# Kernel optimization log

Hardware: AMD Instinct MI355X
Metric: run time of the kernel (lower is better)

## Reference

```python
import jax, jax.numpy as jnp
import numpy as np

N = 50000
E = 800000
EC = 200000
L = 128
PD = 3
IN_MAIN = 2 * L + 2 * (PD + 1)   # 264
IN_CONT = 2 * L + PD + 1          # 260
IN_NODE = 3 * L                   # 384
EPS = 1e-5


def _ln(h):
    # LayerNorm over last dim, no affine params
    m = jnp.mean(h, axis=-1, keepdims=True)
    v = jnp.mean(jnp.square(h - m), axis=-1, keepdims=True)
    return (h - m) * jax.lax.rsqrt(v + EPS)


def _mlp(h, W0, b0, W1, b1, W2, b2):
    # 2 hidden ReLU layers + output Linear + LayerNorm(no affine)
    h = jax.nn.relu(h @ W0 + b0)
    h = jax.nn.relu(h @ W1 + b1)
    return _ln(h @ W2 + b2)


def _mp(x, idx, pos, pos_w, use_mat, W0, b0, W1, b1, W2, b2):
    i, j = idx[0], idx[1]
    x_i = x[i]
    x_j = x[j]
    feats = []
    if use_mat:
        d = pos[i] - pos[j]
        feats += [d, jnp.linalg.norm(d, axis=-1, keepdims=True)]
    dw = pos_w[i] - pos_w[j]
    feats += [dw, jnp.linalg.norm(dw, axis=-1, keepdims=True)]
    tmp = jnp.concatenate(feats + [x_i, x_j], axis=-1)
    emb = _mlp(tmp, W0, b0, W1, b1, W2, b2)
    return jax.ops.segment_sum(emb, j, num_segments=N)


def _lin(key, fan_in, fan_out):
    k1, k2 = jax.random.split(key)
    bd = 1.0 / np.sqrt(fan_in)
    W = jax.random.uniform(k1, (fan_in, fan_out), jnp.float32, -bd, bd)
    b = jax.random.uniform(k2, (fan_out,), jnp.float32, -bd, bd)
    return W, b


def setup_inputs() -> dict:
    key = jax.random.key(0)
    ks = jax.random.split(key, 16)
    inp = {
        "x": jax.random.normal(ks[0], (N, L), jnp.float32),
        "g": jax.random.randint(ks[1], (2, E), 0, N, jnp.int32),
        "cg": jax.random.randint(ks[2], (2, EC), 0, N, jnp.int32),
        "pos_posw": jax.random.normal(ks[3], (N, 2 * PD), jnp.float32),
    }
    dims = {"main": IN_MAIN, "cont": IN_CONT, "node": IN_NODE}
    kidx = 4
    for name, in_dim in dims.items():
        fi = in_dim
        for l in range(3):
            W, b = _lin(ks[kidx], fi, L)
            inp[f"{name}_W{l}"] = W
            inp[f"{name}_b{l}"] = b
            fi = L
            kidx += 1
    return inp


def reference(x, g, cg, pos_posw,
              main_W0, main_b0, main_W1, main_b1, main_W2, main_b2,
              cont_W0, cont_b0, cont_W1, cont_b1, cont_W2, cont_b2,
              node_W0, node_b0, node_W1, node_b1, node_W2, node_b2):
    D = pos_posw.shape[-1] // 2
    pos, pos_w = pos_posw[:, :D], pos_posw[:, D:]
    agg_main = _mp(x, g, pos, pos_w, True,
                   main_W0, main_b0, main_W1, main_b1, main_W2, main_b2)
    agg_cont = _mp(x, cg, pos, pos_w, False,
                   cont_W0, cont_b0, cont_W1, cont_b1, cont_W2, cont_b2)
    tmp = jnp.concatenate([x, agg_main, agg_cont], axis=-1)
    return _mlp(tmp, node_W0, node_b0, node_W1, node_b1, node_W2, node_b2) + x
```

## Files before the change

### kernel.cpp

```cpp
#include <hip/hip_runtime.h>

#define NN 50000
#define NE_MAIN 800000
#define NE_CONT 200000
#define NP 50176

typedef __attribute__((ext_vector_type(8))) short bf8;
typedef __attribute__((ext_vector_type(4))) float f4;

static __device__ __forceinline__ float bf2f(short s) {
  return __builtin_bit_cast(float, ((unsigned int)(unsigned short)s) << 16);
}
static __device__ __forceinline__ short f2bf(float f) {
  unsigned int u = __builtin_bit_cast(unsigned int, f);
  u += 0x7fffu + ((u >> 16) & 1u);
  return (short)(u >> 16);
}

static __device__ __forceinline__ int xcd_swizzle(int bid, int nwg) {
  int xcd = bid & 7;
  int q = nwg >> 3, r = nwg & 7;
  int base = (xcd < r) ? xcd * (q + 1) : r * (q + 1) + (xcd - r) * q;
  return base + (bid >> 3);
}

__global__ __launch_bounds__(256) void zero_kernel(f4* __restrict__ p, int n4) {
  int i = blockIdx.x * 256 + threadIdx.x;
  int stride = gridDim.x * 256;
  f4 z = {0.f, 0.f, 0.f, 0.f};
  for (; i < n4; i += stride) p[i] = z;
}

__global__ __launch_bounds__(256) void hist_kernel(const int* __restrict__ idx, int nE,
                                                   int* __restrict__ hist) {
  int e = blockIdx.x * 256 + threadIdx.x;
  int st = gridDim.x * 256;
  for (; e < nE; e += st) atomicAdd(&hist[idx[nE + e]], 1);
}

__global__ __launch_bounds__(512) void scan1_kernel(const int* __restrict__ hist,
                                                    int* __restrict__ cursor,
                                                    int* __restrict__ tsums, int n) {
  __shared__ int buf[2][512];
  int tid = threadIdx.x;
  int i = blockIdx.x * 512 + tid;
  int v = (i < n) ? hist[i] : 0;
  int cur = 0;
  buf[0][tid] = v;
  __syncthreads();
#pragma unroll
  for (int off = 1; off < 512; off <<= 1) {
    int t = buf[cur][tid];
    if (tid >= off) t += buf[cur][tid - off];
    buf[cur ^ 1][tid] = t;
    cur ^= 1;
    __syncthreads();
  }
  int incl = buf[cur][tid];
  if (i < n) cursor[i] = incl - v;
  if (tid == 511) tsums[blockIdx.x] = incl;
}

__global__ __launch_bounds__(512) void scan2_kernel(int* __restrict__ tsums, int nt) {
  __shared__ int buf[2][512];
  int tid = threadIdx.x;
  int v = (tid < nt) ? tsums[tid] : 0;
  int cur = 0;
  buf[0][tid] = v;
  __syncthreads();
#pragma unroll
  for (int off = 1; off < 512; off <<= 1) {
    int t = buf[cur][tid];
    if (tid >= off) t += buf[cur][tid - off];
    buf[cur ^ 1][tid] = t;
    cur ^= 1;
    __syncthreads();
  }
  if (tid < nt) tsums[tid] = buf[cur][tid] - v;
}

__global__ __launch_bounds__(512) void scan3_kernel(int* __restrict__ cursor,
                                                    const int* __restrict__ tsums, int n) {
  int i = blockIdx.x * 512 + threadIdx.x;
  if (i < n) cursor[i] += tsums[blockIdx.x];
}

__global__ __launch_bounds__(256) void scatter_kernel(const int* __restrict__ idx, int nE,
                                                      int* __restrict__ cursor,
                                                      int* __restrict__ si, int* __restrict__ sj) {
  int e = blockIdx.x * 256 + threadIdx.x;
  int st = gridDim.x * 256;
  for (; e < nE; e += st) {
    int i = idx[e], j = idx[nE + e];
    int p = atomicAdd(&cursor[j], 1);
    si[p] = i;
    sj[p] = j;
  }
}

struct WTDesc {
  const float* src[11];
  int K[11];
  int off[11];
};
__global__ __launch_bounds__(128) void wt_kernel(WTDesc d, short* __restrict__ dst) {
  int m = blockIdx.x >> 7;
  int n = blockIdx.x & 127;
  const float* s = d.src[m];
  int K = d.K[m];
  short* o = dst + d.off[m] + (size_t)n * K;
  for (int k = threadIdx.x; k < K; k += 128) o[k] = f2bf(s[(size_t)k * 128 + n]);
}

template <int K>
static __device__ __forceinline__ void mfma_gemm(const short* __restrict__ sA, int rs16,
                                                 const short* __restrict__ WT,
                                                 int c0, int lane,
                                                 const float* __restrict__ bias,
                                                 f4 (&acc)[4][2]) {
  const int colA = c0 + (lane & 15);
  const int colB = colA + 16;
  if (bias) {
    float ba = bias[colA], bb = bias[colB];
#pragma unroll
    for (int rf = 0; rf < 4; ++rf) {
      acc[rf][0] = (f4){ba, ba, ba, ba};
      acc[rf][1] = (f4){bb, bb, bb, bb};
    }
  } else {
#pragma unroll
    for (int rf = 0; rf < 4; ++rf) {
      acc[rf][0] = (f4){0.f, 0.f, 0.f, 0.f};
      acc[rf][1] = (f4){0.f, 0.f, 0.f, 0.f};
    }
  }
  const int g = lane >> 4;
  const int rowl = lane & 15;
#pragma unroll 4
  for (int ks = 0; ks < (K >> 5); ++ks) {
    bf8 b0 = *reinterpret_cast<const bf8*>(WT + (size_t)colA * K + ks * 32 + g * 8);
    bf8 b1 = *reinterpret_cast<const bf8*>(WT + (size_t)colB * K + ks * 32 + g * 8);
    int chunk = ks * 4 + g;
#pragma unroll
    for (int rf = 0; rf < 4; ++rf) {
      int row = rf * 16 + rowl;
      bf8 a = *reinterpret_cast<const bf8*>(sA + row * rs16 * 8 + ((chunk ^ (row & 7)) << 3));
      acc[rf][0] = __builtin_amdgcn_mfma_f32_16x16x32_bf16(a, b0, acc[rf][0], 0, 0, 0);
      acc[rf][1] = __builtin_amdgcn_mfma_f32_16x16x32_bf16(a, b1, acc[rf][1], 0, 0, 0);
    }
  }
}

template <bool RELU, bool SWZ>
static __device__ __forceinline__ void store_frags(short* __restrict__ dst, int rs16,
                                                   int c0, int lane, const f4 (&acc)[4][2]) {
#pragma unroll
  for (int rf = 0; rf < 4; ++rf)
#pragma unroll
    for (int q = 0; q < 4; ++q) {
      int row = rf * 16 + ((lane >> 4) << 2) + q;
#pragma unroll
      for (int cf = 0; cf < 2; ++cf) {
        int col = c0 + cf * 16 + (lane & 15);
        float v = acc[rf][cf][q];
        if (RELU) v = fmaxf(v, 0.f);
        int idx;
        if (SWZ) idx = row * rs16 * 8 + (((col >> 3) ^ (row & 7)) << 3) + (col & 7);
        else     idx = row * rs16 * 8 + col;
        dst[idx] = f2bf(v);
      }
    }
}

static __device__ __forceinline__ void ln_rows(const f4 (&acc)[4][2], int lane, int wave,
                                               float2* __restrict__ sP) {
#pragma unroll
  for (int rf = 0; rf < 4; ++rf)
#pragma unroll
    for (int q = 0; q < 4; ++q) {
      float v0 = acc[rf][0][q], v1 = acc[rf][1][q];
      float s = v0 + v1;
      float qq = v0 * v0 + v1 * v1;
      s += __shfl_xor(s, 1);  qq += __shfl_xor(qq, 1);
      s += __shfl_xor(s, 2);  qq += __shfl_xor(qq, 2);
      s += __shfl_xor(s, 4);  qq += __shfl_xor(qq, 4);
      s += __shfl_xor(s, 8);  qq += __shfl_xor(qq, 8);
      if ((lane & 15) == 0) {
        int row = rf * 16 + ((lane >> 4) << 2) + q;
        sP[wave * 64 + row] = make_float2(s, qq);
      }
    }
}

__global__ __launch_bounds__(256) void precompute_kernel(
    const float* __restrict__ x, const short* __restrict__ WTp,
    short* __restrict__ xa_m, short* __restrict__ xb_m,
    short* __restrict__ xa_c, short* __restrict__ xb_c) {
  __shared__ __align__(16) short sA[64 * 128];
  __shared__ __align__(16) short sOut[64 * 128];
  const int tid = threadIdx.x;
  const int lane = tid & 63, wave = tid >> 6;
  const int c0 = wave * 32;
  const int n0 = blockIdx.x * 64;

#pragma unroll
  for (int it = 0; it < 4; ++it) {
    int s = it * 256 + tid;
    int e = s >> 4, c = s & 15;
    int n = n0 + e;
    f4 u0 = {0.f, 0.f, 0.f, 0.f}, u1 = {0.f, 0.f, 0.f, 0.f};
    if (n < NN) {
      u0 = *reinterpret_cast<const f4*>(x + (size_t)n * 128 + c * 8);
      u1 = *reinterpret_cast<const f4*>(x + (size_t)n * 128 + c * 8 + 4);
    }
    bf8 o;
#pragma unroll
    for (int j = 0; j < 4; ++j) { o[j] = f2bf(u0[j]); o[j + 4] = f2bf(u1[j]); }
    *reinterpret_cast<bf8*>(sA + e * 128 + ((c ^ (e & 7)) << 3)) = o;
  }
  __syncthreads();

  short* dsts[4] = {xa_m, xb_m, xa_c, xb_c};
#pragma unroll 1
  for (int o = 0; o < 4; ++o) {
    f4 acc[4][2];
    mfma_gemm<128>(sA, 16, WTp + o * 16384, c0, lane, nullptr, acc);
    store_frags<false, false>(sOut, 16, c0, lane, acc);
    __syncthreads();
    short* dst = dsts[o];
#pragma unroll
    for (int it = 0; it < 4; ++it) {
      int s = it * 256 + tid;
      int e = s >> 4, c = s & 15;
      int n = n0 + e;
      if (n < NN)
        *reinterpret_cast<bf8*>(dst + (size_t)n * 128 + c * 8) =
            *reinterpret_cast<const bf8*>(sOut + e * 128 + c * 8);
    }
    __syncthreads();
  }
}

template <int NF>
__global__ __launch_bounds__(256) void edge_kernel(
    const int* __restrict__ si, const int* __restrict__ sjv, int nE,
    const float* __restrict__ pp,
    const short* __restrict__ xa, const short* __restrict__ xb,
    const float* __restrict__ W0f, const float* __restrict__ b0v,
    const short* __restrict__ WT1, const float* __restrict__ b1v,
    const short* __restrict__ WT2, const float* __restrict__ b2v,
    float* __restrict__ agg) {
  __shared__ __align__(16) short sAB[2 * 64 * 128];
  __shared__ int sI[64], sJ[64];
  __shared__ float sF[64][NF];
  __shared__ float2 sP[4 * 64];
  __shared__ float2 sStats[64];
  const int tid = threadIdx.x;
  const int lane = tid & 63, wave = tid >> 6;
  const int c0 = wave * 32;
  const int base = xcd_swizzle(blockIdx.x, gridDim.x) * 64;
  short* sA = sAB;
  short* sB = sAB + 64 * 128;
  float* sT = reinterpret_cast<float*>(sAB);

  if (tid < 64) {
    int e = base + tid;
    int i = si[e];
    int j = sjv[e];
    sI[tid] = i; sJ[tid] = j;
    const float* pi = pp + (size_t)i * 6;
    const float* pj = pp + (size_t)j * 6;
    if (NF == 8) {
      float d0 = pi[0] - pj[0], d1 = pi[1] - pj[1], d2 = pi[2] - pj[2];
      sF[tid][0] = d0; sF[tid][1] = d1; sF[tid][2] = d2;
      sF[tid][3] = sqrtf(d0 * d0 + d1 * d1 + d2 * d2);
      float w0 = pi[3] - pj[3], w1 = pi[4] - pj[4], w2 = pi[5] - pj[5];
      sF[tid][4] = w0; sF[tid][5] = w1; sF[tid][6] = w2;
      sF[tid][7] = sqrtf(w0 * w0 + w1 * w1 + w2 * w2);
    } else {
      float w0 = pi[3] - pj[3], w1 = pi[4] - pj[4], w2 = pi[5] - pj[5];
      sF[tid][0] = w0; sF[tid][1] = w1; sF[tid][2] = w2;
      sF[tid][3] = sqrtf(w0 * w0 + w1 * w1 + w2 * w2);
    }
  }
  __syncthreads();

#pragma unroll
  for (int it = 0; it < 4; ++it) {
    int s = it * 256 + tid;
    int e = s >> 4, c = s & 15;
    int i = sI[e], j = sJ[e];
    bf8 va = *reinterpret_cast<const bf8*>(xa + (size_t)i * 128 + c * 8);
    bf8 vb = *reinterpret_cast<const bf8*>(xb + (size_t)j * 128 + c * 8);
    f4 b0a = *reinterpret_cast<const f4*>(b0v + c * 8);
    f4 b0b = *reinterpret_cast<const f4*>(b0v + c * 8 + 4);
    float h[8];
#pragma unroll
    for (int jj = 0; jj < 4; ++jj) {
      h[jj]     = bf2f(va[jj])     + bf2f(vb[jj])     + b0a[jj];
      h[jj + 4] = bf2f(va[jj + 4]) + bf2f(vb[jj + 4]) + b0b[jj];
    }
#pragma unroll
    for (int q = 0; q < NF; ++q) {
      float fq = sF[e][q];
      f4 w0 = *reinterpret_cast<const f4*>(W0f + q * 128 + c * 8);
      f4 w1 = *reinterpret_cast<const f4*>(W0f + q * 128 + c * 8 + 4);
#pragma unroll
      for (int jj = 0; jj < 4; ++jj) {
        h[jj]     = fmaf(fq, w0[jj], h[jj]);
        h[jj + 4] = fmaf(fq, w1[jj], h[jj + 4]);
      }
    }
    bf8 o;
#pragma unroll
    for (int jj = 0; jj < 8; ++jj) o[jj] = f2bf(fmaxf(h[jj], 0.f));
    *reinterpret_cast<bf8*>(sA + e * 128 + ((c ^ (e & 7)) << 3)) = o;
  }
  __syncthreads();

  f4 acc[4][2];
  mfma_gemm<128>(sA, 16, WT1, c0, lane, b1v, acc);
  store_frags<true, true>(sB, 16, c0, lane, acc);
  __syncthreads();
  mfma_gemm<128>(sB, 16, WT2, c0, lane, b2v, acc);

  ln_rows(acc, lane, wave, sP);
  __syncthreads();
  if (tid < 64) {
    float s = 0.f, qq = 0.f;
#pragma unroll
    for (int w = 0; w < 4; ++w) { s += sP[w * 64 + tid].x; qq += sP[w * 64 + tid].y; }
    float mean = s * (1.f / 128.f);
    float var = qq * (1.f / 128.f) - mean * mean;
    sStats[tid] = make_float2(mean, rsqrtf(var + 1e-5f));
  }
  __syncthreads();

#pragma unroll
  for (int rf = 0; rf < 4; ++rf)
#pragma unroll
    for (int q = 0; q < 4; ++q) {
      int row = rf * 16 + ((lane >> 4) << 2) + q;
      float mean = sStats[row].x, rn = sStats[row].y;
#pragma unroll
      for (int cf = 0; cf < 2; ++cf) {
        int col = c0 + cf * 16 + (lane & 15);
        sT[row * 128 + col] = (acc[rf][cf][q] - mean) * rn;
      }
    }
  __syncthreads();

  {
    int grp = tid >> 7, c = tid & 127;
    int r0 = grp * 32;
    float accum = 0.f;
#pragma unroll 4
    for (int r = r0; r < r0 + 32; ++r) {
      accum += sT[r * 128 + c];
      bool flush = (r == r0 + 31) || (sJ[r + 1] != sJ[r]);
      if (flush) {
        unsafeAtomicAdd(agg + (size_t)sJ[r] * 128 + c, accum);
        accum = 0.f;
      }
    }
  }
}

__global__ __launch_bounds__(256) void node_kernel(
    const float* __restrict__ x,
    const float* __restrict__ agg_m, const float* __restrict__ agg_c,
    const short* __restrict__ WT0, const float* __restrict__ b0v,
    const short* __restrict__ WT1, const float* __restrict__ b1v,
    const short* __restrict__ WT2, const float* __restrict__ b2v,
    float* __restrict__ out) {
  __shared__ __align__(16) short sA[64 * 384];
  __shared__ float2 sP[4 * 64];
  __shared__ float2 sStats[64];
  const int tid = threadIdx.x;
  const int lane = tid & 63, wave = tid >> 6;
  const int c0 = wave * 32;
  const int n0 = blockIdx.x * 64;

#pragma unroll
  for (int p = 0; p < 3; ++p) {
    const float* src = (p == 0) ? x : (p == 1) ? agg_m : agg_c;
#pragma unroll
    for (int it = 0; it < 4; ++it) {
      int s = it * 256 + tid;
      int e = s >> 4, cl = s & 15;
      int n = n0 + e;
      f4 u0 = {0.f, 0.f, 0.f, 0.f}, u1 = {0.f, 0.f, 0.f, 0.f};
      if (n < NN) {
        u0 = *reinterpret_cast<const f4*>(src + (size_t)n * 128 + cl * 8);
        u1 = *reinterpret_cast<const f4*>(src + (size_t)n * 128 + cl * 8 + 4);
      }
      bf8 o;
#pragma unroll
      for (int j = 0; j < 4; ++j) { o[j] = f2bf(u0[j]); o[j + 4] = f2bf(u1[j]); }
      int c = p * 16 + cl;
      *reinterpret_cast<bf8*>(sA + e * 384 + ((c ^ (e & 7)) << 3)) = o;
    }
  }
  __syncthreads();

  f4 acc[4][2];
  mfma_gemm<384>(sA, 48, WT0, c0, lane, b0v, acc);
  __syncthreads();
  store_frags<true, true>(sA, 16, c0, lane, acc);
  __syncthreads();
  mfma_gemm<128>(sA, 16, WT1, c0, lane, b1v, acc);
  __syncthreads();
  store_frags<true, true>(sA + 8192, 16, c0, lane, acc);
  __syncthreads();
  mfma_gemm<128>(sA + 8192, 16, WT2, c0, lane, b2v, acc);

  ln_rows(acc, lane, wave, sP);
  __syncthreads();
  if (tid < 64) {
    float s = 0.f, qq = 0.f;
#pragma unroll
    for (int w = 0; w < 4; ++w) { s += sP[w * 64 + tid].x; qq += sP[w * 64 + tid].y; }
    float mean = s * (1.f / 128.f);
    float var = qq * (1.f / 128.f) - mean * mean;
    sStats[tid] = make_float2(mean, rsqrtf(var + 1e-5f));
  }
  __syncthreads();

#pragma unroll
  for (int rf = 0; rf < 4; ++rf)
#pragma unroll
    for (int q = 0; q < 4; ++q) {
      int row = rf * 16 + ((lane >> 4) << 2) + q;
      int n = n0 + row;
      if (n < NN) {
        float mean = sStats[row].x, rn = sStats[row].y;
#pragma unroll
        for (int cf = 0; cf < 2; ++cf) {
          int col = c0 + cf * 16 + (lane & 15);
          float xv = x[(size_t)n * 128 + col];
          out[(size_t)n * 128 + col] = (acc[rf][cf][q] - mean) * rn + xv;
        }
      }
    }
}

extern "C" void kernel_launch(void* const* d_in, const int* in_sizes, int n_in,
                              void* d_out, int out_size, void* d_ws, size_t ws_size,
                              hipStream_t stream) {
  const float* x   = (const float*)d_in[0];
  const int*   g   = (const int*)d_in[1];
  const int*   cgr = (const int*)d_in[2];
  const float* pp  = (const float*)d_in[3];
  const float* mW0 = (const float*)d_in[4];
  const float* mb0 = (const float*)d_in[5];
  const float* mW1 = (const float*)d_in[6];
  const float* mb1 = (const float*)d_in[7];
  const float* mW2 = (const float*)d_in[8];
  const float* mb2 = (const float*)d_in[9];
  const float* cW0 = (const float*)d_in[10];
  const float* cb0 = (const float*)d_in[11];
  const float* cW1 = (const float*)d_in[12];
  const float* cb1 = (const float*)d_in[13];
  const float* cW2 = (const float*)d_in[14];
  const float* cb2 = (const float*)d_in[15];
  const float* nW0 = (const float*)d_in[16];
  const float* nb0 = (const float*)d_in[17];
  const float* nW1 = (const float*)d_in[18];
  const float* nb1 = (const float*)d_in[19];
  const float* nW2 = (const float*)d_in[20];
  const float* nb2 = (const float*)d_in[21];
  float* out = (float*)d_out;

  WTDesc d;
  const float* srcs[11] = {mW1, mW2, cW1, cW2, nW0, nW1, nW2,
                           mW0 + 8 * 128, mW0 + 136 * 128, cW0 + 4 * 128, cW0 + 132 * 128};
  int Ks[11] = {128, 128, 128, 128, 384, 128, 128, 128, 128, 128, 128};
  int off = 0;
  for (int m = 0; m < 11; ++m) { d.src[m] = srcs[m]; d.K[m] = Ks[m]; d.off[m] = off; off += Ks[m] * 128; }

  char* ws = (char*)d_ws;
  const size_t TBL = (size_t)NN * 128 * 2;
  const size_t AGG = (size_t)NN * 128 * 4;
  short* xa_m = (short*)(ws);
  short* xb_m = (short*)(ws + TBL);
  short* xa_c = (short*)(ws + 2 * TBL);
  short* xb_c = (short*)(ws + 3 * TBL);
  float* agg_m = (float*)(ws + 4 * TBL);
  float* agg_c = (float*)(ws + 4 * TBL + AGG);
  short* wt = (short*)(ws + 4 * TBL + 2 * AGG);
  char* ib = ws + 4 * TBL + 2 * AGG + (size_t)off * 2;
  int* hist_m   = (int*)(ib);
  int* hist_c   = hist_m + NP;
  int* cursor_m = hist_c + NP;
  int* cursor_c = cursor_m + NP;
  int* tsum_m   = cursor_c + NP;
  int* tsum_c   = tsum_m + 128;
  int* si_m     = tsum_c + 128;
  int* sj_m     = si_m + NE_MAIN;
  int* si_c     = sj_m + NE_MAIN;
  int* sj_c     = si_c + NE_CONT;

  short* wt1_m = wt + d.off[0];
  short* wt2_m = wt + d.off[1];
  short* wt1_c = wt + d.off[2];
  short* wt2_c = wt + d.off[3];
  short* wtn0  = wt + d.off[4];
  short* wtn1  = wt + d.off[5];
  short* wtn2  = wt + d.off[6];
  short* wtp   = wt + d.off[7];

  const int NT = (NN + 511) / 512;

  wt_kernel<<<11 * 128, 128, 0, stream>>>(d, wt);
  zero_kernel<<<2048, 256, 0, stream>>>((f4*)agg_m, (int)(2 * (size_t)NN * 128 / 4));
  zero_kernel<<<128, 256, 0, stream>>>((f4*)hist_m, 2 * NP / 4);

  hist_kernel<<<1024, 256, 0, stream>>>(g, NE_MAIN, hist_m);
  hist_kernel<<<512, 256, 0, stream>>>(cgr, NE_CONT, hist_c);
  scan1_kernel<<<NT, 512, 0, stream>>>(hist_m, cursor_m, tsum_m, NN);
  scan1_kernel<<<NT, 512, 0, stream>>>(hist_c, cursor_c, tsum_c, NN);
  scan2_kernel<<<1, 512, 0, stream>>>(tsum_m, NT);
  scan2_kernel<<<1, 512, 0, stream>>>(tsum_c, NT);
  scan3_kernel<<<NT, 512, 0, stream>>>(cursor_m, tsum_m, NN);
  scan3_kernel<<<NT, 512, 0, stream>>>(cursor_c, tsum_c, NN);
  scatter_kernel<<<1024, 256, 0, stream>>>(g, NE_MAIN, cursor_m, si_m, sj_m);
  scatter_kernel<<<512, 256, 0, stream>>>(cgr, NE_CONT, cursor_c, si_c, sj_c);

  precompute_kernel<<<(NN + 63) / 64, 256, 0, stream>>>(x, wtp, xa_m, xb_m, xa_c, xb_c);
  edge_kernel<8><<<NE_MAIN / 64, 256, 0, stream>>>(si_m, sj_m, NE_MAIN, pp, xa_m, xb_m,
                                                   mW0, mb0, wt1_m, mb1, wt2_m, mb2, agg_m);
  edge_kernel<4><<<NE_CONT / 64, 256, 0, stream>>>(si_c, sj_c, NE_CONT, pp, xa_c, xb_c,
                                                   cW0, cb0, wt1_c, cb1, wt2_c, cb2, agg_c);
  node_kernel<<<(NN + 63) / 64, 256, 0, stream>>>(x, agg_m, agg_c,
                                                  wtn0, nb0, wtn1, nb1, wtn2, nb2, out);
}
```

Before: 670.6 us.

## Fuse edge kernels into persistent kernel with prefetched gathers and bias folding

Result: slower. 1.097 ms (+63.5%).

```diff
diff --git a/kernel.cpp b/kernel.cpp
--- a/kernel.cpp
+++ b/kernel.cpp
@@ -1,9 +1,12 @@
 #include <hip/hip_runtime.h>
+#include <hip/hip_bf16.h>
 
 #define NN 50000
 #define NE_MAIN 800000
 #define NE_CONT 200000
 #define NP 50176
+#define BLK_M 768
+#define BLK_C 192
 
 typedef __attribute__((ext_vector_type(8))) short bf8;
 typedef __attribute__((ext_vector_type(4))) float f4;
@@ -12,16 +15,8 @@
   return __builtin_bit_cast(float, ((unsigned int)(unsigned short)s) << 16);
 }
 static __device__ __forceinline__ short f2bf(float f) {
-  unsigned int u = __builtin_bit_cast(unsigned int, f);
-  u += 0x7fffu + ((u >> 16) & 1u);
-  return (short)(u >> 16);
-}
-
-static __device__ __forceinline__ int xcd_swizzle(int bid, int nwg) {
-  int xcd = bid & 7;
-  int q = nwg >> 3, r = nwg & 7;
-  int base = (xcd < r) ? xcd * (q + 1) : r * (q + 1) + (xcd - r) * q;
-  return base + (bid >> 3);
+  __hip_bfloat16 h = __float2bfloat16(f);
+  return __builtin_bit_cast(short, h);
 }
 
 __global__ __launch_bounds__(256) void zero_kernel(f4* __restrict__ p, int n4) {
@@ -194,6 +189,7 @@
 
 __global__ __launch_bounds__(256) void precompute_kernel(
     const float* __restrict__ x, const short* __restrict__ WTp,
+    const float* __restrict__ mb0, const float* __restrict__ cb0,
     short* __restrict__ xa_m, short* __restrict__ xb_m,
     short* __restrict__ xa_c, short* __restrict__ xb_c) {
   __shared__ __align__(16) short sA[64 * 128];
@@ -221,10 +217,11 @@
   __syncthreads();
 
   short* dsts[4] = {xa_m, xb_m, xa_c, xb_c};
+  const float* biases[4] = {nullptr, mb0, nullptr, cb0};
 #pragma unroll 1
   for (int o = 0; o < 4; ++o) {
     f4 acc[4][2];
-    mfma_gemm<128>(sA, 16, WTp + o * 16384, c0, lane, nullptr, acc);
+    mfma_gemm<128>(sA, 16, WTp + o * 16384, c0, lane, biases[o], acc);
     store_frags<false, false>(sOut, 16, c0, lane, acc);
     __syncthreads();
     short* dst = dsts[o];
@@ -241,128 +238,180 @@
   }
 }
 
+struct EdgeArgs {
+  const int* si; const int* sj;
+  const short* xa; const short* xb;
+  const float* pp;
+  const float* W0f;
+  const short* WT1; const float* b1;
+  const short* WT2; const float* b2;
+  float* agg;
+  int ntiles; int nblocks; int nf;
+};
+
 template <int NF>
-__global__ __launch_bounds__(256) void edge_kernel(
-    const int* __restrict__ si, const int* __restrict__ sjv, int nE,
-    const float* __restrict__ pp,
-    const short* __restrict__ xa, const short* __restrict__ xb,
-    const float* __restrict__ W0f, const float* __restrict__ b0v,
-    const short* __restrict__ WT1, const float* __restrict__ b1v,
-    const short* __restrict__ WT2, const float* __restrict__ b2v,
-    float* __restrict__ agg) {
+static __device__ __forceinline__ void stage_h0(short* __restrict__ sA,
+                                                const bf8 (&pxa)[4], const bf8 (&pxb)[4],
+                                                const float (* __restrict__ sFc)[8],
+                                                const float* __restrict__ W0f, int tid) {
+#pragma unroll
+  for (int it = 0; it < 4; ++it) {
+    int s = it * 256 + tid;
+    int e = s >> 4, c = s & 15;
+    float h[8];
+#pragma unroll
+    for (int jj = 0; jj < 8; ++jj) h[jj] = bf2f(pxa[it][jj]) + bf2f(pxb[it][jj]);
+#pragma unroll
+    for (int q = 0; q < NF; ++q) {
+      float fq = sFc[e][q];
+      f4 w0 = *reinterpret_cast<const f4*>(W0f + q * 128 + c * 8);
+      f4 w1 = *reinterpret_cast<const f4*>(W0f + q * 128 + c * 8 + 4);
+#pragma unroll
+      for (int jj = 0; jj < 4; ++jj) {
+        h[jj]     = fmaf(fq, w0[jj], h[jj]);
+        h[jj + 4] = fmaf(fq, w1[jj], h[jj + 4]);
+      }
+    }
+    bf8 o;
+#pragma unroll
+    for (int jj = 0; jj < 8; ++jj) o[jj] = f2bf(fmaxf(h[jj], 0.f));
+    *reinterpret_cast<bf8*>(sA + e * 128 + ((c ^ (e & 7)) << 3)) = o;
+  }
+}
+
+__global__ __launch_bounds__(256, 4) void edge_fused_kernel(EdgeArgs am, EdgeArgs ac,
+                                                            int blocks_m) {
   __shared__ __align__(16) short sAB[2 * 64 * 128];
-  __shared__ int sI[64], sJ[64];
-  __shared__ float sF[64][NF];
+  __shared__ int sI[2][64], sJ[2][64];
+  __shared__ float sF[2][64][8];
   __shared__ float2 sP[4 * 64];
   __shared__ float2 sStats[64];
   const int tid = threadIdx.x;
   const int lane = tid & 63, wave = tid >> 6;
   const int c0 = wave * 32;
-  const int base = xcd_swizzle(blockIdx.x, gridDim.x) * 64;
   short* sA = sAB;
   short* sB = sAB + 64 * 128;
   float* sT = reinterpret_cast<float*>(sAB);
 
+  EdgeArgs A;
+  int lb;
+  if ((int)blockIdx.x < blocks_m) { A = am; lb = blockIdx.x; }
+  else                            { A = ac; lb = blockIdx.x - blocks_m; }
+  const int per = A.nblocks >> 3;
+  lb = (lb & 7) * per + (lb >> 3);
+  const int q = A.ntiles / A.nblocks, r = A.ntiles % A.nblocks;
+  const int t0 = lb * q + (lb < r ? lb : r);
+  const int t1 = t0 + q + (lb < r ? 1 : 0);
+  if (t0 >= t1) return;
+  const int nf = A.nf;
+
+  int cur = 0;
   if (tid < 64) {
-    int e = base + tid;
-    int i = si[e];
-    int j = sjv[e];
-    sI[tid] = i; sJ[tid] = j;
-    const float* pi = pp + (size_t)i * 6;
-    const float* pj = pp + (size_t)j * 6;
-    if (NF == 8) {
+    int e = t0 * 64 + tid;
+    int i = A.si[e], j = A.sj[e];
+    sI[0][tid] = i; sJ[0][tid] = j;
+    const float* pi = A.pp + (size_t)i * 6;
+    const float* pj = A.pp + (size_t)j * 6;
+    float d0 = pi[0] - pj[0], d1 = pi[1] - pj[1], d2 = pi[2] - pj[2];
+    float w0 = pi[3] - pj[3], w1 = pi[4] - pj[4], w2 = pi[5] - pj[5];
+    float* sf = sF[0][tid];
+    if (nf == 8) {
+      sf[0] = d0; sf[1] = d1; sf[2] = d2; sf[3] = sqrtf(d0 * d0 + d1 * d1 + d2 * d2);
+      sf[4] = w0; sf[5] = w1; sf[6] = w2; sf[7] = sqrtf(w0 * w0 + w1 * w1 + w2 * w2);
+    } else {
+      sf[0] = w0; sf[1] = w1; sf[2] = w2; sf[3] = sqrtf(w0 * w0 + w1 * w1 + w2 * w2);
+    }
+  }
+  __syncthreads();
+
+  bf8 pxa[4], pxb[4];
+#pragma unroll
+  for (int it = 0; it < 4; ++it) {
+    int s = it * 256 + tid, e = s >> 4, c = s & 15;
+    pxa[it] = *reinterpret_cast<const bf8*>(A.xa + (size_t)sI[0][e] * 128 + c * 8);
+    pxb[it] = *reinterpret_cast<const bf8*>(A.xb + (size_t)sJ[0][e] * 128 + c * 8);
+  }
+
+  for (int tt = t0; tt < t1; ++tt) {
+    const bool nb = (tt + 1 < t1);
+    int ni = 0, nj2 = 0;
+    if (nb && tid < 64) {
+      int e = (tt + 1) * 64 + tid;
+      ni = A.si[e];
+      nj2 = A.sj[e];
+    }
+    if (nf == 8) stage_h0<8>(sA, pxa, pxb, sF[cur], A.W0f, tid);
+    else         stage_h0<4>(sA, pxa, pxb, sF[cur], A.W0f, tid);
+    __syncthreads();
+    if (nb && tid < 64) {
+      int nxt = cur ^ 1;
+      sI[nxt][tid] = ni; sJ[nxt][tid] = nj2;
+      const float* pi = A.pp + (size_t)ni * 6;
+      const float* pj = A.pp + (size_t)nj2 * 6;
       float d0 = pi[0] - pj[0], d1 = pi[1] - pj[1], d2 = pi[2] - pj[2];
-      sF[tid][0] = d0; sF[tid][1] = d1; sF[tid][2] = d2;
-      sF[tid][3] = sqrtf(d0 * d0 + d1 * d1 + d2 * d2);
       float w0 = pi[3] - pj[3], w1 = pi[4] - pj[4], w2 = pi[5] - pj[5];
-      sF[tid][4] = w0; sF[tid][5] = w1; sF[tid][6] = w2;
-      sF[tid][7] = sqrtf(w0 * w0 + w1 * w1 + w2 * w2);
-    } else {
-      float w0 = pi[3] - pj[3], w1 = pi[4] - pj[4], w2 = pi[5] - pj[5];
-      sF[tid][0] = w0; sF[tid][1] = w1; sF[tid][2] = w2;
-      sF[tid][3] = sqrtf(w0 * w0 + w1 * w1 + w2 * w2);
-    }
-  }
-  __syncthreads();
-
-#pragma unroll
-  for (int it = 0; it < 4; ++it) {
-    int s = it * 256 + tid;
-    int e = s >> 4, c = s & 15;
-    int i = sI[e], j = sJ[e];
-    bf8 va = *reinterpret_cast<const bf8*>(xa + (size_t)i * 128 + c * 8);
-    bf8 vb = *reinterpret_cast<const bf8*>(xb + (size_t)j * 128 + c * 8);
-    f4 b0a = *reinterpret_cast<const f4*>(b0v + c * 8);
-    f4 b0b = *reinterpret_cast<const f4*>(b0v + c * 8 + 4);
-    float h[8];
-#pragma unroll
-    for (int jj = 0; jj < 4; ++jj) {
-      h[jj]     = bf2f(va[jj])     + bf2f(vb[jj])     + b0a[jj];
-      h[jj + 4] = bf2f(va[jj + 4]) + bf2f(vb[jj + 4]) + b0b[jj];
-    }
-#pragma unroll
-    for (int q = 0; q < NF; ++q) {
-      float fq = sF[e][q];
-      f4 w0 = *reinterpret_cast<const f4*>(W0f + q * 128 + c * 8);
-      f4 w1 = *reinterpret_cast<const f4*>(W0f + q * 128 + c * 8 + 4);
-#pragma unroll
-      for (int jj = 0; jj < 4; ++jj) {
-        h[jj]     = fmaf(fq, w0[jj], h[jj]);
-        h[jj + 4] = fmaf(fq, w1[jj], h[jj + 4]);
-      }
-    }
-    bf8 o;
-#pragma unroll
-    for (int jj = 0; jj < 8; ++jj) o[jj] = f2bf(fmaxf(h[jj], 0.f));
-    *reinterpret_cast<bf8*>(sA + e * 128 + ((c ^ (e & 7)) << 3)) = o;
-  }
-  __syncthreads();
-
-  f4 acc[4][2];
-  mfma_gemm<128>(sA, 16, WT1, c0, lane, b1v, acc);
-  store_frags<true, true>(sB, 16, c0, lane, acc);
-  __syncthreads();
-  mfma_gemm<128>(sB, 16, WT2, c0, lane, b2v, acc);
-
-  ln_rows(acc, lane, wave, sP);
-  __syncthreads();
-  if (tid < 64) {
-    float s = 0.f, qq = 0.f;
-#pragma unroll
-    for (int w = 0; w < 4; ++w) { s += sP[w * 64 + tid].x; qq += sP[w * 64 + tid].y; }
-    float mean = s * (1.f / 128.f);
-    float var = qq * (1.f / 128.f) - mean * mean;
-    sStats[tid] = make_float2(mean, rsqrtf(var + 1e-5f));
-  }
-  __syncthreads();
-
-#pragma unroll
-  for (int rf = 0; rf < 4; ++rf)
-#pragma unroll
-    for (int q = 0; q < 4; ++q) {
-      int row = rf * 16 + ((lane >> 4) << 2) + q;
-      float mean = sStats[row].x, rn = sStats[row].y;
-#pragma unroll
-      for (int cf = 0; cf < 2; ++cf) {
-        int col = c0 + cf * 16 + (lane & 15);
-        sT[row * 128 + col] = (acc[rf][cf][q] - mean) * rn;
-      }
-    }
-  __syncthreads();
-
-  {
-    int grp = tid >> 7, c = tid & 127;
-    int r0 = grp * 32;
-    float accum = 0.f;
+      float* sf = sF[nxt][tid];
+      if (nf == 8) {
+        sf[0] = d0; sf[1] = d1; sf[2] = d2; sf[3] = sqrtf(d0 * d0 + d1 * d1 + d2 * d2);
+        sf[4] = w0; sf[5] = w1; sf[6] = w2; sf[7] = sqrtf(w0 * w0 + w1 * w1 + w2 * w2);
+      } else {
+        sf[0] = w0; sf[1] = w1; sf[2] = w2; sf[3] = sqrtf(w0 * w0 + w1 * w1 + w2 * w2);
+      }
+    }
+    f4 acc[4][2];
+    mfma_gemm<128>(sA, 16, A.WT1, c0, lane, A.b1, acc);
+    store_frags<true, true>(sB, 16, c0, lane, acc);
+    __syncthreads();
+    if (nb) {
+      int nxt = cur ^ 1;
+#pragma unroll
+      for (int it = 0; it < 4; ++it) {
+        int s = it * 256 + tid, e = s >> 4, c = s & 15;
+        pxa[it] = *reinterpret_cast<const bf8*>(A.xa + (size_t)sI[nxt][e] * 128 + c * 8);
+        pxb[it] = *reinterpret_cast<const bf8*>(A.xb + (size_t)sJ[nxt][e] * 128 + c * 8);
+      }
+    }
+    mfma_gemm<128>(sB, 16, A.WT2, c0, lane, A.b2, acc);
+    ln_rows(acc, lane, wave, sP);
+    __syncthreads();
+    if (tid < 64) {
+      float s = 0.f, qq = 0.f;
+#pragma unroll
+      for (int w = 0; w < 4; ++w) { s += sP[w * 64 + tid].x; qq += sP[w * 64 + tid].y; }
+      float mean = s * (1.f / 128.f);
+      float var = qq * (1.f / 128.f) - mean * mean;
+      sStats[tid] = make_float2(mean, rsqrtf(var + 1e-5f));
+    }
+    __syncthreads();
+#pragma unroll
+    for (int rf = 0; rf < 4; ++rf)
+#pragma unroll
+      for (int qq2 = 0; qq2 < 4; ++qq2) {
+        int row = rf * 16 + ((lane >> 4) << 2) + qq2;
+        float mean = sStats[row].x, rn = sStats[row].y;
+#pragma unroll
+        for (int cf = 0; cf < 2; ++cf) {
+          int col = c0 + cf * 16 + (lane & 15);
+          sT[row * 128 + ((col + 4 * row) & 127)] = (acc[rf][cf][qq2] - mean) * rn;
+        }
+      }
+    __syncthreads();
+    {
+      int grp = tid >> 7, c = tid & 127;
+      int r0g = grp * 32;
+      float accum = 0.f;
 #pragma unroll 4
-    for (int r = r0; r < r0 + 32; ++r) {
-      accum += sT[r * 128 + c];
-      bool flush = (r == r0 + 31) || (sJ[r + 1] != sJ[r]);
-      if (flush) {
-        unsafeAtomicAdd(agg + (size_t)sJ[r] * 128 + c, accum);
-        accum = 0.f;
-      }
-    }
+      for (int rr = r0g; rr < r0g + 32; ++rr) {
+        accum += sT[rr * 128 + ((c + 4 * rr) & 127)];
+        bool flush = (rr == r0g + 31) || (sJ[cur][rr + 1] != sJ[cur][rr]);
+        if (flush) {
+          unsafeAtomicAdd(A.agg + (size_t)sJ[cur][rr] * 128 + c, accum);
+          accum = 0.f;
+        }
+      }
+    }
+    __syncthreads();
+    cur ^= 1;
   }
 }
 
@@ -526,11 +575,15 @@
   scatter_kernel<<<1024, 256, 0, stream>>>(g, NE_MAIN, cursor_m, si_m, sj_m);
   scatter_kernel<<<512, 256, 0, stream>>>(cgr, NE_CONT, cursor_c, si_c, sj_c);
 
-  precompute_kernel<<<(NN + 63) / 64, 256, 0, stream>>>(x, wtp, xa_m, xb_m, xa_c, xb_c);
-  edge_kernel<8><<<NE_MAIN / 64, 256, 0, stream>>>(si_m, sj_m, NE_MAIN, pp, xa_m, xb_m,
-                                                   mW0, mb0, wt1_m, mb1, wt2_m, mb2, agg_m);
-  edge_kernel<4><<<NE_CONT / 64, 256, 0, stream>>>(si_c, sj_c, NE_CONT, pp, xa_c, xb_c,
-                                                   cW0, cb0, wt1_c, cb1, wt2_c, cb2, agg_c);
+  precompute_kernel<<<(NN + 63) / 64, 256, 0, stream>>>(x, wtp, mb0, cb0,
+                                                        xa_m, xb_m, xa_c, xb_c);
+
+  EdgeArgs am = {si_m, sj_m, xa_m, xb_m, pp, mW0, wt1_m, mb1, wt2_m, mb2,
+                 agg_m, NE_MAIN / 64, BLK_M, 8};
+  EdgeArgs ac = {si_c, sj_c, xa_c, xb_c, pp, cW0, wt1_c, cb1, wt2_c, cb2,
+                 agg_c, NE_CONT / 64, BLK_C, 4};
+  edge_fused_kernel<<<BLK_M + BLK_C, 256, 0, stream>>>(am, ac, BLK_M);
+
   node_kernel<<<(NN + 63) / 64, 256, 0, stream>>>(x, agg_m, agg_c,
                                                   wtn0, nb0, wtn1, nb1, wtn2, nb2, out);
 }
```
